# Optimization experiments

Measured on AMD Instinct MI355X. Metric: run time of the kernel, lower is better.

Reference implementation:

```python
import jax, jax.numpy as jnp
import numpy as np

IN_DIMS = [3, 16, 16]
OUT_DIMS = [16, 16, 3]
GRID_SIZE = 8
SPLINE_ORDER = 3
GRID_RANGE = (-1.0, 1.0)
K = GRID_SIZE + SPLINE_ORDER  # number of B-spline basis functions = 11

# extended knot grid, identical for every feature (as in standard KAN layers)
_h = (GRID_RANGE[1] - GRID_RANGE[0]) / GRID_SIZE
GRID_NP = np.arange(-SPLINE_ORDER, GRID_SIZE + SPLINE_ORDER + 1, dtype=np.float32) * _h + GRID_RANGE[0]

# per-layer parameter slice boundaries: [coef, univariate_weight, residual_weight] per layer
_sizes = [0]
for di, do in zip(IN_DIMS, OUT_DIMS):
    _sizes.extend([di * do * K, di * do, di * do])
PARAM_IDX = np.cumsum(_sizes)
KAN_PARAMS_NUM = int(PARAM_IDX[-1])  # 4576


def bspline_basis(x, grid):
    """Cox-de Boor recursion. x: [...,], grid: [G]. Returns [..., K]."""
    x = x[..., None]
    b = ((x >= grid[:-1]) & (x < grid[1:])).astype(x.dtype)
    for p in range(1, SPLINE_ORDER + 1):
        left = (x - grid[:-(p + 1)]) / (grid[p:-1] - grid[:-(p + 1)]) * b[..., :-1]
        right = (grid[p + 1:] - x) / (grid[p + 1:] - grid[1:-p]) * b[..., 1:]
        b = left + right
    return b  # [..., GRID_SIZE + SPLINE_ORDER]


def setup_inputs() -> dict:
    key = jax.random.key(0)
    k1, k2, k3, k4 = jax.random.split(key, 4)
    B, C, H, W = 8, 3, 224, 224
    x = jax.random.uniform(k1, (B, C, H, W), dtype=jnp.float32)  # in grid range
    features = jax.random.normal(k2, (B, 1000), dtype=jnp.float32)  # resnet18 output stand-in
    fc_w = jax.random.normal(k3, (KAN_PARAMS_NUM, 1000), dtype=jnp.float32) * 0.02
    fc_b = jax.random.normal(k4, (KAN_PARAMS_NUM,), dtype=jnp.float32) * 0.02
    return {"x": x, "features": features, "fc_w": fc_w, "fc_b": fc_b}


def reference(x, features, fc_w, fc_b):
    B, C, H, W = x.shape
    # hypernetwork head: per-sample flat KAN parameter vector [B, P]
    w = features @ fc_w.T + fc_b
    # image -> per-pixel tokens [B, T, C]
    y = jnp.transpose(x, (0, 2, 3, 1)).reshape(B, H * W, C)
    grid = jnp.asarray(GRID_NP, dtype=x.dtype)
    for n, (di, do) in enumerate(zip(IN_DIMS, OUT_DIMS)):
        i0, i1, i2, i3 = PARAM_IDX[3 * n: 3 * n + 4]
        coef = w[:, i0:i1].reshape(B, di, do, K)       # spline coefficients
        uw = w[:, i1:i2].reshape(B, di, do)            # univariate (spline) weight
        rw = w[:, i2:i3].reshape(B, di, do)            # residual (silu) weight
        basis = bspline_basis(y, grid)                 # [B, T, di, K]
        spline = jnp.einsum('btik,biok->bto', basis, coef * uw[..., None])
        base = jnp.einsum('bti,bio->bto', jax.nn.silu(y), rw)
        y = spline + base                              # [B, T, do]
    out = y.reshape(B, H, W, -1)
    return jnp.transpose(out, (0, 3, 1, 2))
```

## Files before the change

kernel.cpp:

```cpp
#include <hip/hip_runtime.h>

#define HW   50176
#define NPAR 4576

typedef _Float16 half8 __attribute__((ext_vector_type(8)));
typedef __attribute__((ext_vector_type(4))) float f32x4;
typedef __attribute__((ext_vector_type(4))) int int4v;

__device__ __forceinline__ unsigned short f2h(float f) {
    union { _Float16 h; unsigned short u; } c; c.h = (_Float16)f; return c.u;
}
__device__ __forceinline__ float h2f(unsigned short u) {
    union { _Float16 h; unsigned short u; } c; c.u = u; return (float)c.h;
}

__global__ __launch_bounds__(64) void gemm_w(const float* __restrict__ feats,
                                             const float* __restrict__ fcw,
                                             const float* __restrict__ fcb,
                                             float* __restrict__ wout) {
    int lane = threadIdx.x, nn = lane & 15, quad = lane >> 4;
    int n = blockIdx.x * 16 + nn;
    const float* brow = fcw + (size_t)n * 1000;
    const float* arow = feats + nn * 1000;

    f32x4 acc = {0.f, 0.f, 0.f, 0.f};
#pragma unroll 2
    for (int s = 0; s < 32; s++) {
        int kb = s * 32 + quad * 8;
        float4 a0 = {0,0,0,0}, a1 = {0,0,0,0}, b0 = {0,0,0,0}, b1 = {0,0,0,0};
        if (kb < 1000) {
            b0 = *(const float4*)(brow + kb);
            b1 = *(const float4*)(brow + kb + 4);
            if (nn < 8) {
                a0 = *(const float4*)(arow + kb);
                a1 = *(const float4*)(arow + kb + 4);
            }
        }
        float af[8] = {a0.x, a0.y, a0.z, a0.w, a1.x, a1.y, a1.z, a1.w};
        float bf[8] = {b0.x, b0.y, b0.z, b0.w, b1.x, b1.y, b1.z, b1.w};
        half8 ah, al, bh;
#pragma unroll
        for (int j = 0; j < 8; j++) {
            ah[j] = (_Float16)af[j];
            al[j] = (_Float16)(af[j] - (float)ah[j]);
            bh[j] = (_Float16)bf[j];
        }
        acc = __builtin_amdgcn_mfma_f32_16x16x32_f16(ah, bh, acc, 0, 0, 0);
        acc = __builtin_amdgcn_mfma_f32_16x16x32_f16(al, bh, acc, 0, 0, 0);
    }
    if (quad < 2) {
        float bias = fcb[n];
#pragma unroll
        for (int r = 0; r < 4; r++)
            wout[(size_t)(quad * 4 + r) * NPAR + n] = acc[r] + bias;
    }
}

__global__ __launch_bounds__(256) void pack_b(const float* __restrict__ w,
                                              unsigned int* __restrict__ bt) {
    int idx = blockIdx.x * 256 + threadIdx.x;
    if (idx >= 8 * 4608) return;
    int b = idx / 4608, r = idx - b * 4608;
    int ks = r >> 8, ln = (r >> 2) & 63, dq = r & 3;
    int q = ln >> 4, n = ln & 15;
    int lay, s;
    if (ks < 2)       { lay = 0; s = ks; }
    else if (ks < 10) { lay = 1; s = ks - 2; }
    else              { lay = 2; s = ks - 10; }
    int i = 2 * s + (q >> 1);
    const float* wb = w + b * NPAR;
    int cb, ub, rb2, nd, ni;
    if (lay == 0)      { cb = 0;    ub = 528;  rb2 = 576;  nd = 16; ni = 3;  }
    else if (lay == 1) { cb = 624;  ub = 3440; rb2 = 3696; nd = 16; ni = 16; }
    else               { cb = 3952; ub = 4480; rb2 = 4528; nd = 3;  ni = 16; }
    unsigned int pk = 0;
    if (i < ni && n < nd) {
        float uwv = wb[ub + i * nd + n];
        float rwv = wb[rb2 + i * nd + n];
        unsigned short rh = f2h(rwv);
        float rl = rwv - h2f(rh);
#pragma unroll
        for (int h = 0; h < 2; h++) {
            int rk = (q & 1) * 8 + dq * 2 + h;
            float v = 0.f;
            if (rk < 11)       v = wb[cb + (i * nd + n) * 11 + rk] * uwv;
            else if (rk < 13)  v = rwv;
            else if (rk == 13) v = rl;
            pk |= ((unsigned int)f2h(v)) << (16 * h);
        }
    }
    bt[idx] = pk;
}

__device__ __forceinline__ void scatter_row(int* g0, int* g1, float y) {
    float t  = (y + 1.75f) * 4.0f;
    float ft = floorf(t);
    ft = fminf(fmaxf(ft, -8.0f), 24.0f);
    int jt  = (int)ft;
    float u = t - ft;
    float u2 = u * u, u3 = u2 * u, om = 1.0f - u;
    float b0 = (1.0f / 6.0f) * om * om * om;
    float b3 = (1.0f / 6.0f) * u3;
    float b1 = 0.5f * u3 - u2 + (2.0f / 3.0f);
    float b2 = 1.0f - b0 - b1 - b3;
    float sil = y / (1.0f + __expf(-y));
    unsigned short sh = f2h(sil);
    float sl = sil - h2f(sh);
    float t10 = 0.f;
    t10 = (jt == 13) ? b0 : t10;
    t10 = (jt == 12) ? b1 : t10;
    t10 = (jt == 11) ? b2 : t10;
    t10 = (jt == 10) ? b3 : t10;
    int4v z = {0, 0, 0, 0};
    int4v w1;
    w1[0] = 0;
    w1[1] = (int)((unsigned int)f2h(t10) | ((unsigned int)sh << 16));
    w1[2] = (int)((unsigned int)f2h(sl)  | ((unsigned int)sh << 16));
    w1[3] = 0;
    *(int4v*)g0 = z;
    *(int4v*)g1 = w1;
    int r0 = jt - 3;
    unsigned short hb0 = f2h(b0), hb1 = f2h(b1), hb2 = f2h(b2), hb3 = f2h(b3);
#pragma unroll
    for (int j = 0; j < 4; j++) {
        int s = r0 + j;
        unsigned short hv = (j == 0) ? hb0 : (j == 1) ? hb1 : (j == 2) ? hb2 : hb3;
        if ((unsigned)s <= 10u) {
            short* sp = (s < 8) ? (short*)g0 : (short*)g1;
            sp[s & 7] = (short)hv;
        }
    }
}

#define YBOFF 4096

__global__ __launch_bounds__(256) void kan_mfma(const float* __restrict__ x,
                                                const unsigned int* __restrict__ bt,
                                                float* __restrict__ out) {
    __shared__ __align__(16) int lds[YBOFF + 256 * 17];
    const int tid  = threadIdx.x;
    const int lane = tid & 63, wave = tid >> 6;
    const int quad = lane >> 4, nn = lane & 15;
    const int b = blockIdx.x / 196;
    const int px0 = (blockIdx.x - b * 196) * 256;
    const unsigned int* btb = bt + b * 4608;
    float* ybf = (float*)&lds[YBOFF];

    int* slice = &lds[wave * 1024];
    int* gp[4];
#pragma unroll
    for (int g = 0; g < 4; g++)
        gp[g] = slice + lane * 16 + ((((lane >> 1) + g) & 3) * 4);

    const int rot = (((nn >> 1) + quad) & 3) * 4;
    const int aob = wave * 1024 + nn * 16 + rot;

    const float* xg = x + (size_t)b * 3 * HW + px0 + tid;
    float xv0 = xg[0], xv1 = xg[HW], xv2 = xg[2 * HW];

    f32x4 acc[4];

    auto kstep = [&](int ks) {
        union { half8 h; int4v v; } bf;
        bf.v = *(const int4v*)(btb + ks * 256 + lane * 4);
        asm volatile("s_waitcnt lgkmcnt(0)" ::: "memory");
#pragma unroll
        for (int mt = 0; mt < 4; mt++) {
            union { half8 h; int4v v; } af;
            af.v = *(int4v*)&lds[aob + mt * 256];
            acc[mt] = __builtin_amdgcn_mfma_f32_16x16x32_f16(af.h, bf.h, acc[mt], 0, 0, 0);
        }
        asm volatile("" ::: "memory");
    };

#pragma unroll
    for (int mt = 0; mt < 4; mt++) acc[mt] = (f32x4){0.f, 0.f, 0.f, 0.f};
    scatter_row(gp[0], gp[1], xv0);
    scatter_row(gp[2], gp[3], xv1);
    kstep(0);
    scatter_row(gp[0], gp[1], xv2);
    kstep(1);
#pragma unroll
    for (int mt = 0; mt < 4; mt++)
#pragma unroll
        for (int r = 0; r < 4; r++)
            ybf[(wave * 64 + mt * 16 + quad * 4 + r) * 17 + nn] = acc[mt][r];
    asm volatile("s_waitcnt lgkmcnt(0)" ::: "memory");

#pragma unroll
    for (int mt = 0; mt < 4; mt++) acc[mt] = (f32x4){0.f, 0.f, 0.f, 0.f};
#pragma unroll 1
    for (int s = 0; s < 8; s++) {
        float y0 = ybf[tid * 17 + 2 * s];
        float y1 = ybf[tid * 17 + 2 * s + 1];
        scatter_row(gp[0], gp[1], y0);
        scatter_row(gp[2], gp[3], y1);
        kstep(2 + s);
    }
#pragma unroll
    for (int mt = 0; mt < 4; mt++)
#pragma unroll
        for (int r = 0; r < 4; r++)
            ybf[(wave * 64 + mt * 16 + quad * 4 + r) * 17 + nn] = acc[mt][r];
    asm volatile("s_waitcnt lgkmcnt(0)" ::: "memory");

#pragma unroll
    for (int mt = 0; mt < 4; mt++) acc[mt] = (f32x4){0.f, 0.f, 0.f, 0.f};
#pragma unroll 1
    for (int s = 0; s < 8; s++) {
        float y0 = ybf[tid * 17 + 2 * s];
        float y1 = ybf[tid * 17 + 2 * s + 1];
        scatter_row(gp[0], gp[1], y0);
        scatter_row(gp[2], gp[3], y1);
        kstep(10 + s);
    }

    if (nn < 3) {
#pragma unroll
        for (int mt = 0; mt < 4; mt++)
#pragma unroll
            for (int r = 0; r < 4; r++)
                ybf[(wave * 64 + mt * 16 + quad * 4 + r) * 17 + nn] = acc[mt][r];
    }
    asm volatile("s_waitcnt lgkmcnt(0)" ::: "memory");
    float c0 = ybf[tid * 17 + 0];
    float c1 = ybf[tid * 17 + 1];
    float c2 = ybf[tid * 17 + 2];
    float* ob = out + (size_t)b * 3 * HW + px0 + tid;
    ob[0]      = c0;
    ob[HW]     = c1;
    ob[2 * HW] = c2;
}

extern "C" void kernel_launch(void* const* d_in, const int* in_sizes, int n_in,
                              void* d_out, int out_size, void* d_ws, size_t ws_size,
                              hipStream_t stream) {
    const float* x     = (const float*)d_in[0];
    const float* feats = (const float*)d_in[1];
    const float* fcw   = (const float*)d_in[2];
    const float* fcb   = (const float*)d_in[3];
    float* outp = (float*)d_out;
    float* wbuf = (float*)d_ws;
    unsigned int* btens = (unsigned int*)d_ws + 36608;

    hipLaunchKernelGGL(gemm_w, dim3(286), dim3(64), 0, stream,
                       feats, fcw, fcb, wbuf);
    hipLaunchKernelGGL(pack_b, dim3(144), dim3(256), 0, stream,
                       wbuf, btens);
    hipLaunchKernelGGL(kan_mfma, dim3(8 * 196), dim3(256), 0, stream,
                       x, btens, outp);
}
```

Baseline: 129.6 us.

## Split gemm_w K-loop across four waves with LDS reduction; simplify basis scatter

```diff
diff --git a/kernel.cpp b/kernel.cpp
--- a/kernel.cpp
+++ b/kernel.cpp
@@ -14,19 +14,21 @@
     union { _Float16 h; unsigned short u; } c; c.u = u; return (float)c.h;
 }
 
-__global__ __launch_bounds__(64) void gemm_w(const float* __restrict__ feats,
-                                             const float* __restrict__ fcw,
-                                             const float* __restrict__ fcb,
-                                             float* __restrict__ wout) {
-    int lane = threadIdx.x, nn = lane & 15, quad = lane >> 4;
+__global__ __launch_bounds__(256) void gemm_w(const float* __restrict__ feats,
+                                              const float* __restrict__ fcw,
+                                              const float* __restrict__ fcb,
+                                              float* __restrict__ wout) {
+    __shared__ float red[4][64][4];
+    int tid = threadIdx.x, lane = tid & 63, wave = tid >> 6;
+    int nn = lane & 15, quad = lane >> 4;
     int n = blockIdx.x * 16 + nn;
     const float* brow = fcw + (size_t)n * 1000;
     const float* arow = feats + nn * 1000;
 
     f32x4 acc = {0.f, 0.f, 0.f, 0.f};
-#pragma unroll 2
-    for (int s = 0; s < 32; s++) {
-        int kb = s * 32 + quad * 8;
+#pragma unroll 4
+    for (int s8 = 0; s8 < 8; s8++) {
+        int kb = (wave * 8 + s8) * 32 + quad * 8;
         float4 a0 = {0,0,0,0}, a1 = {0,0,0,0}, b0 = {0,0,0,0}, b1 = {0,0,0,0};
         if (kb < 1000) {
             b0 = *(const float4*)(brow + kb);
@@ -48,11 +50,17 @@
         acc = __builtin_amdgcn_mfma_f32_16x16x32_f16(ah, bh, acc, 0, 0, 0);
         acc = __builtin_amdgcn_mfma_f32_16x16x32_f16(al, bh, acc, 0, 0, 0);
     }
-    if (quad < 2) {
+#pragma unroll
+    for (int r = 0; r < 4; r++) red[wave][lane][r] = acc[r];
+    __syncthreads();
+    if (wave == 0 && quad < 2) {
         float bias = fcb[n];
 #pragma unroll
-        for (int r = 0; r < 4; r++)
-            wout[(size_t)(quad * 4 + r) * NPAR + n] = acc[r] + bias;
+        for (int r = 0; r < 4; r++) {
+            float v = red[0][lane][r] + red[1][lane][r]
+                    + red[2][lane][r] + red[3][lane][r];
+            wout[(size_t)(quad * 4 + r) * NPAR + n] = v + bias;
+        }
     }
 }
 
@@ -106,29 +114,22 @@
     float sil = y / (1.0f + __expf(-y));
     unsigned short sh = f2h(sil);
     float sl = sil - h2f(sh);
-    float t10 = 0.f;
-    t10 = (jt == 13) ? b0 : t10;
-    t10 = (jt == 12) ? b1 : t10;
-    t10 = (jt == 11) ? b2 : t10;
-    t10 = (jt == 10) ? b3 : t10;
     int4v z = {0, 0, 0, 0};
     int4v w1;
     w1[0] = 0;
-    w1[1] = (int)((unsigned int)f2h(t10) | ((unsigned int)sh << 16));
-    w1[2] = (int)((unsigned int)f2h(sl)  | ((unsigned int)sh << 16));
+    w1[1] = (int)((unsigned int)sh << 16);
+    w1[2] = (int)((unsigned int)f2h(sl) | ((unsigned int)sh << 16));
     w1[3] = 0;
     *(int4v*)g0 = z;
     *(int4v*)g1 = w1;
     int r0 = jt - 3;
-    unsigned short hb0 = f2h(b0), hb1 = f2h(b1), hb2 = f2h(b2), hb3 = f2h(b3);
+    unsigned short hb[4] = {f2h(b0), f2h(b1), f2h(b2), f2h(b3)};
 #pragma unroll
     for (int j = 0; j < 4; j++) {
         int s = r0 + j;
-        unsigned short hv = (j == 0) ? hb0 : (j == 1) ? hb1 : (j == 2) ? hb2 : hb3;
-        if ((unsigned)s <= 10u) {
-            short* sp = (s < 8) ? (short*)g0 : (short*)g1;
-            sp[s & 7] = (short)hv;
-        }
+        int slot = ((unsigned)s <= 10u) ? s : 15;
+        short* sp = (short*)((slot < 8) ? g0 : g1);
+        sp[slot & 7] = (short)hb[j];
     }
 }
 
@@ -243,7 +244,7 @@
     float* wbuf = (float*)d_ws;
     unsigned int* btens = (unsigned int*)d_ws + 36608;
 
-    hipLaunchKernelGGL(gemm_w, dim3(286), dim3(64), 0, stream,
+    hipLaunchKernelGGL(gemm_w, dim3(286), dim3(256), 0, stream,
                        feats, fcw, fcb, wbuf);
     hipLaunchKernelGGL(pack_b, dim3(144), dim3(256), 0, stream,
                        wbuf, btens);
```

Result: faster. 116.3 us (-10.3%).
